# Kernel tuning notes

Measured on AMD Instinct MI355X. Metric: run time of the kernel, lower is better.

## Reference

```python
import jax, jax.numpy as jnp
import numpy as np

EMBED = 1024
HEADS = 16
HEAD_DIM = EMBED // HEADS
FFN = 4096
BSZ = 2
CHUNK = 128
NCHUNK = 16
REG_LEN = CHUNK * NCHUNK   # 2048
SUM_LEN = NCHUNK           # 1 summary token per chunk
NEG = -1e9


def _layer_norm(x, g, b, eps=1e-5):
    mu = x.mean(-1, keepdims=True)
    var = ((x - mu) ** 2).mean(-1, keepdims=True)
    return (x - mu) * jax.lax.rsqrt(var + eps) * g + b


def _build_mask(reg_chunk_ranges, sum_len, reg_len):
    # True = attention allowed. Museformer hierarchical scheme:
    #   rr: reg token attends reg tokens of its OWN chunk, causally
    #   rs: reg token attends summary tokens of STRICTLY EARLIER chunks
    #   sr: summary token of chunk c attends reg tokens of chunk c
    #   ss: causal among summary tokens
    bsz = reg_chunk_ranges.shape[0]
    starts = reg_chunk_ranges[:, :, 0]                       # [B, C]
    t = jnp.arange(reg_len)
    chunk_id = (t[None, :, None] >= starts[:, None, :]).sum(-1) - 1   # [B, R]
    sum_chunk = jnp.arange(sum_len)                          # [S]
    rr = (chunk_id[:, :, None] == chunk_id[:, None, :]) & (t[None, :, None] >= t[None, None, :])
    rs = sum_chunk[None, None, :] < chunk_id[:, :, None]     # [B, R, S]
    sr = chunk_id[:, None, :] == sum_chunk[None, :, None]    # [B, S, R]
    ss = jnp.broadcast_to(sum_chunk[:, None] >= sum_chunk[None, :], (bsz, sum_len, sum_len))
    top = jnp.concatenate([ss, sr], axis=2)
    bot = jnp.concatenate([rs, rr], axis=2)
    return jnp.concatenate([top, bot], axis=1)               # [B, S+R, S+R]


def _forward(x, w_q, w_k, w_v, w_o,
             ln_sa_sum_g, ln_sa_sum_b, ln_sa_reg_g, ln_sa_reg_b,
             sum_fc1_w, sum_fc1_b, sum_fc2_w, sum_fc2_b,
             reg_fc1_w, reg_fc1_b, reg_fc2_w, reg_fc2_b,
             ln_f_sum_g, ln_f_sum_b, ln_f_reg_g, ln_f_reg_b,
             reg_chunk_ranges, sum_len, reg_len):
    bsz, total, d = x.shape
    # --- self-attention block (pre-norm, separate LN for sum/reg parts) ---
    hs = _layer_norm(x[:, :sum_len], ln_sa_sum_g, ln_sa_sum_b)
    hr = _layer_norm(x[:, sum_len:], ln_sa_reg_g, ln_sa_reg_b)
    h = jnp.concatenate([hs, hr], axis=1)
    q = (h @ w_q.T).reshape(bsz, total, HEADS, HEAD_DIM)
    k = (h @ w_k.T).reshape(bsz, total, HEADS, HEAD_DIM)
    v = (h @ w_v.T).reshape(bsz, total, HEADS, HEAD_DIM)
    scores = jnp.einsum('bqhd,bkhd->bhqk', q, k) * (HEAD_DIM ** -0.5)
    mask = _build_mask(reg_chunk_ranges, sum_len, reg_len)   # [B, T, T] bool
    scores = jnp.where(mask[:, None], scores, NEG)
    attn = jax.nn.softmax(scores, axis=-1)
    ctx = jnp.einsum('bhqk,bkhd->bqhd', attn, v).reshape(bsz, total, d)
    x = x + ctx @ w_o.T
    # --- FFN block (pre-norm, separate LN/FFN for sum/reg parts) ---
    fs = _layer_norm(x[:, :sum_len], ln_f_sum_g, ln_f_sum_b)
    fs = jax.nn.relu(fs @ sum_fc1_w.T + sum_fc1_b) @ sum_fc2_w.T + sum_fc2_b
    fr = _layer_norm(x[:, sum_len:], ln_f_reg_g, ln_f_reg_b)
    fr = jax.nn.relu(fr @ reg_fc1_w.T + reg_fc1_b) @ reg_fc2_w.T + reg_fc2_b
    return x + jnp.concatenate([fs, fr], axis=1)


def setup_inputs() -> dict:
    key = jax.random.key(0)
    ks = jax.random.split(key, 12)
    s = 0.02
    total = SUM_LEN + REG_LEN
    starts = (np.arange(NCHUNK) * CHUNK).astype(np.int32)
    ranges = np.stack([starts, starts + CHUNK], axis=-1)     # [C, 2]
    reg_chunk_ranges = jnp.asarray(np.broadcast_to(ranges, (BSZ, NCHUNK, 2)).copy())
    d = dict(
        x=jax.random.normal(ks[0], (BSZ, total, EMBED), jnp.float32),
        w_q=jax.random.normal(ks[1], (EMBED, EMBED), jnp.float32) * s,
        w_k=jax.random.normal(ks[2], (EMBED, EMBED), jnp.float32) * s,
        w_v=jax.random.normal(ks[3], (EMBED, EMBED), jnp.float32) * s,
        w_o=jax.random.normal(ks[4], (EMBED, EMBED), jnp.float32) * s,
        ln_sa_sum_g=jnp.ones((EMBED,)), ln_sa_sum_b=jnp.zeros((EMBED,)),
        ln_sa_reg_g=jnp.ones((EMBED,)), ln_sa_reg_b=jnp.zeros((EMBED,)),
        sum_fc1_w=jax.random.normal(ks[5], (FFN, EMBED), jnp.float32) * s,
        sum_fc1_b=jnp.zeros((FFN,)),
        sum_fc2_w=jax.random.normal(ks[6], (EMBED, FFN), jnp.float32) * s,
        sum_fc2_b=jnp.zeros((EMBED,)),
        reg_fc1_w=jax.random.normal(ks[7], (FFN, EMBED), jnp.float32) * s,
        reg_fc1_b=jnp.zeros((FFN,)),
        reg_fc2_w=jax.random.normal(ks[8], (EMBED, FFN), jnp.float32) * s,
        reg_fc2_b=jnp.zeros((EMBED,)),
        ln_f_sum_g=jnp.ones((EMBED,)), ln_f_sum_b=jnp.zeros((EMBED,)),
        ln_f_reg_g=jnp.ones((EMBED,)), ln_f_reg_b=jnp.zeros((EMBED,)),
        reg_chunk_ranges=reg_chunk_ranges,
        sum_len=SUM_LEN,
        reg_len=REG_LEN,
    )
    return d


def reference(x, w_q, w_k, w_v, w_o,
              ln_sa_sum_g, ln_sa_sum_b, ln_sa_reg_g, ln_sa_reg_b,
              sum_fc1_w, sum_fc1_b, sum_fc2_w, sum_fc2_b,
              reg_fc1_w, reg_fc1_b, reg_fc2_w, reg_fc2_b,
              ln_f_sum_g, ln_f_sum_b, ln_f_reg_g, ln_f_reg_b,
              reg_chunk_ranges, sum_len, reg_len):
    return _forward(x, w_q, w_k, w_v, w_o,
                    ln_sa_sum_g, ln_sa_sum_b, ln_sa_reg_g, ln_sa_reg_b,
                    sum_fc1_w, sum_fc1_b, sum_fc2_w, sum_fc2_b,
                    reg_fc1_w, reg_fc1_b, reg_fc2_w, reg_fc2_b,
                    ln_f_sum_g, ln_f_sum_b, ln_f_reg_g, ln_f_reg_b,
                    reg_chunk_ranges, sum_len, reg_len)
```

## Files before the change

### kernel.cpp

```cpp
#include <hip/hip_runtime.h>
#include <stdint.h>

typedef __attribute__((ext_vector_type(8))) short short8;
typedef __attribute__((ext_vector_type(4))) float f32x4;

__device__ __forceinline__ float bf2f(short s) {
    union { unsigned u; float f; } c;
    c.u = ((unsigned)(unsigned short)s) << 16;
    return c.f;
}
__device__ __forceinline__ short f2bf(float f) {
    union { float f; unsigned u; } c; c.f = f;
    unsigned u = c.u + 0x7fffu + ((c.u >> 16) & 1u);
    return (short)(u >> 16);
}
__device__ __forceinline__ void gll16(const short* g, short* l) {
    __builtin_amdgcn_global_load_lds(
        (const __attribute__((address_space(1))) unsigned int*)g,
        (__attribute__((address_space(3))) unsigned int*)l, 16, 0, 0);
}

__global__ __launch_bounds__(256) void cvt_w(
    const float* __restrict__ wq, const float* __restrict__ wk,
    const float* __restrict__ wv, const float* __restrict__ wo,
    const float* __restrict__ f1s, const float* __restrict__ f2s,
    const float* __restrict__ f1r, const float* __restrict__ f2r,
    short* __restrict__ dst)
{
    size_t i = ((size_t)blockIdx.x * 256 + threadIdx.x) * 4;
    const float* src; size_t off;
    if (i < 4194304) {
        int seg = (int)(i >> 20);
        src = seg == 0 ? wq : seg == 1 ? wk : seg == 2 ? wv : wo;
        off = i & 1048575;
    } else {
        size_t ii = i - 4194304;
        int seg = (int)(ii >> 22);
        src = seg == 0 ? f1s : seg == 1 ? f2s : seg == 2 ? f1r : f2r;
        off = ii & 4194303;
    }
    float4 v = *(const float4*)(src + off);
    short4 o;
    o.x = f2bf(v.x); o.y = f2bf(v.y); o.z = f2bf(v.z); o.w = f2bf(v.w);
    *(short4*)(dst + i) = o;
}

template<int PHASE>
__global__ __launch_bounds__(256) void ln_k(
    const float* __restrict__ xin, const short* __restrict__ Pw, float* __restrict__ x1out,
    const float* __restrict__ g_sum, const float* __restrict__ b_sum,
    const float* __restrict__ g_reg, const float* __restrict__ b_reg,
    short* __restrict__ out_all, short* __restrict__ out_s, short* __restrict__ out_r)
{
    int row = blockIdx.x;
    int b = row / 2064, t = row - b * 2064;
    int tid = threadIdx.x;
    int c = tid * 4;
    size_t base = (size_t)row * 1024 + c;
    float4 v = *(const float4*)(xin + base);
    if (PHASE == 1) {
#pragma unroll
        for (int z = 0; z < 4; ++z) {
            short4 p = *(const short4*)(Pw + (size_t)z * 4227072 + base);
            v.x += bf2f(p.x); v.y += bf2f(p.y);
            v.z += bf2f(p.z); v.w += bf2f(p.w);
        }
        *(float4*)(x1out + base) = v;
    }
    float s = v.x + v.y + v.z + v.w;
#pragma unroll
    for (int off = 1; off < 64; off <<= 1) s += __shfl_xor(s, off);
    __shared__ float red[8];
    if ((tid & 63) == 0) red[tid >> 6] = s;
    __syncthreads();
    float mu = (red[0] + red[1] + red[2] + red[3]) * (1.0f / 1024.0f);
    float a0 = v.x - mu, a1 = v.y - mu, a2 = v.z - mu, a3 = v.w - mu;
    float qq = a0 * a0 + a1 * a1 + a2 * a2 + a3 * a3;
#pragma unroll
    for (int off = 1; off < 64; off <<= 1) qq += __shfl_xor(qq, off);
    if ((tid & 63) == 0) red[4 + (tid >> 6)] = qq;
    __syncthreads();
    float var = (red[4] + red[5] + red[6] + red[7]) * (1.0f / 1024.0f);
    float rs = rsqrtf(var + 1e-5f);
    const float* g  = (t < 16) ? g_sum : g_reg;
    const float* be = (t < 16) ? b_sum : b_reg;
    short4 o;
    o.x = f2bf(a0 * rs * g[c]     + be[c]);
    o.y = f2bf(a1 * rs * g[c + 1] + be[c + 1]);
    o.z = f2bf(a2 * rs * g[c + 2] + be[c + 2]);
    o.w = f2bf(a3 * rs * g[c + 3] + be[c + 3]);
    short* dst;
    if (PHASE == 0) dst = out_all + (size_t)row * 1024;
    else dst = (t < 16) ? (out_s + ((size_t)b * 16 + t) * 1024)
                        : (out_r + ((size_t)b * 2048 + (t - 16)) * 1024);
    *(short4*)(dst + c) = o;
}

template<int MODE>
__global__ __launch_bounds__(256) void gemm_bt(
    const short* __restrict__ A, int M, int K, int klen,
    const short* __restrict__ B0, const short* __restrict__ B1, const short* __restrict__ B2,
    const float* __restrict__ bias,
    void* __restrict__ o0, void* __restrict__ o1, void* __restrict__ o2, int seg)
{
    const int tid = threadIdx.x;
    const int w = tid >> 6, l = tid & 63;
    const int lr = l & 15, lh = l >> 4;
    const int m0 = blockIdx.x * 128;
    int ntile = blockIdx.y, nsel = 0;
    const short* B = B0;
    if (MODE == 0) { nsel = ntile >> 3; ntile &= 7; B = nsel == 0 ? B0 : (nsel == 1 ? B1 : B2); }
    const int n0 = ntile * 128;
    const int wr = (w >> 1) * 64, wc = (w & 1) * 64;
    const int kbase = blockIdx.z * klen;

    __shared__ __align__(16) short As[2 * 4096];
    __shared__ __align__(16) short Bs[2 * 4096];

    const int srow = w * 32 + (l >> 2);
    const int scol = (((l & 3) ^ ((l >> 3) & 3))) * 8;
    int ar0 = m0 + srow;      if (ar0 > M - 1) ar0 = M - 1;
    int ar1 = m0 + srow + 16; if (ar1 > M - 1) ar1 = M - 1;
    const short* ga0 = A + (size_t)ar0 * K + scol + kbase;
    const short* ga1 = A + (size_t)ar1 * K + scol + kbase;
    const short* gb0 = B + (size_t)(n0 + srow) * K + scol + kbase;
    const short* gb1 = B + (size_t)(n0 + srow + 16) * K + scol + kbase;
    const int lofs = (w * 32) * 32;

    const int cbrd = (lh ^ ((lr >> 1) & 3)) * 8;

    f32x4 acc[4][4];
#pragma unroll
    for (int m = 0; m < 4; ++m)
#pragma unroll
        for (int n = 0; n < 4; ++n) acc[m][n] = (f32x4){0.f, 0.f, 0.f, 0.f};

    auto STAGE = [&](int j, int buf) {
        const int k0 = j * 32;
        short* a = As + buf * 4096 + lofs;
        short* b = Bs + buf * 4096 + lofs;
        gll16(ga0 + k0, a);
        gll16(ga1 + k0, a + 512);
        gll16(gb0 + k0, b);
        gll16(gb1 + k0, b + 512);
    };

    const int nk = klen >> 5;
    STAGE(0, 0);
    for (int t = 0; t < nk; ++t) {
        __syncthreads();
        const int cur = (t & 1);
        if (t + 1 < nk) STAGE(t + 1, cur ^ 1);
        const int co = cur << 12;
        short8 af[4], bfr[4];
#pragma unroll
        for (int m = 0; m < 4; ++m)
            af[m] = *(const short8*)(As + co + (wr + m * 16 + lr) * 32 + cbrd);
#pragma unroll
        for (int n = 0; n < 4; ++n)
            bfr[n] = *(const short8*)(Bs + co + (wc + n * 16 + lr) * 32 + cbrd);
#pragma unroll
        for (int m = 0; m < 4; ++m)
#pragma unroll
            for (int n = 0; n < 4; ++n)
                acc[m][n] = __builtin_amdgcn_mfma_f32_16x16x32_bf16(af[m], bfr[n], acc[m][n], 0, 0, 0);
    }

#pragma unroll
    for (int m = 0; m < 4; ++m) {
#pragma unroll
        for (int n = 0; n < 4; ++n) {
            int gc = n0 + wc + n * 16 + lr;
#pragma unroll
            for (int j = 0; j < 4; ++j) {
                int gr = m0 + wr + m * 16 + lh * 4 + j;
                if (gr >= M) continue;
                float val = acc[m][n][j];
                if (MODE == 0) {
                    short* o = (short*)(nsel == 0 ? o0 : (nsel == 1 ? o1 : o2));
                    o[(size_t)gr * 1024 + gc] = f2bf(val);
                } else if (MODE == 1) {
                    float* P = (float*)o0 + (size_t)blockIdx.z * (size_t)seg;
                    P[(size_t)gr * 1024 + gc] = val;
                } else if (MODE == 2) {
                    val += bias[gc];
                    val = val > 0.f ? val : 0.f;
                    ((short*)o0)[(size_t)gr * 4096 + gc] = f2bf(val);
                } else {
                    short* P = (short*)o0 + (size_t)blockIdx.z * (size_t)seg;
                    P[(size_t)gr * 1024 + gc] = f2bf(val);
                }
            }
        }
    }
}

__global__ __launch_bounds__(256) void reduce_f2reg(
    const float* __restrict__ x1, const short* __restrict__ P,
    const float* __restrict__ bias, float* __restrict__ out)
{
    size_t i = ((size_t)blockIdx.x * 256 + threadIdx.x) * 4;
    int gr = (int)(i >> 10), c = (int)(i & 1023);
    size_t g = (size_t)((gr >> 11) * 2064 + 16 + (gr & 2047)) * 1024 + c;
    float4 r  = *(const float4*)(x1 + g);
    float4 bb = *(const float4*)(bias + c);
    float ox = r.x + bb.x, oy = r.y + bb.y, oz = r.z + bb.z, ow = r.w + bb.w;
#pragma unroll
    for (int z = 0; z < 4; ++z) {
        short4 p = *(const short4*)(P + (size_t)z * 4194304 + i);
        ox += bf2f(p.x); oy += bf2f(p.y); oz += bf2f(p.z); ow += bf2f(p.w);
    }
    float4 o; o.x = ox; o.y = oy; o.z = oz; o.w = ow;
    *(float4*)(out + g) = o;
}

__global__ __launch_bounds__(256) void reduce_f2sum(
    const float* __restrict__ x1, const float* __restrict__ P,
    const float* __restrict__ bias, float* __restrict__ out)
{
    int i = (blockIdx.x * 256 + threadIdx.x) * 4;
    int gr = i >> 10, c = i & 1023;
    size_t g = (size_t)((gr >> 4) * 2064 + (gr & 15)) * 1024 + c;
    float4 r  = *(const float4*)(x1 + g);
    float4 bb = *(const float4*)(bias + c);
    float ox = r.x + bb.x, oy = r.y + bb.y, oz = r.z + bb.z, ow = r.w + bb.w;
#pragma unroll
    for (int s = 0; s < 16; ++s) {
        float4 p = *(const float4*)(P + s * 32768 + i);
        ox += p.x; oy += p.y; oz += p.z; ow += p.w;
    }
    float4 o; o.x = ox; o.y = oy; o.z = oz; o.w = ow;
    *(float4*)(out + g) = o;
}

__global__ __launch_bounds__(256) void attn_reg(
    const short* __restrict__ q, const short* __restrict__ k,
    const short* __restrict__ v, short* __restrict__ ctx)
{
    __shared__ __align__(16) short Pl[128 * 168];
    __shared__ __align__(16) short Vt[64 * 168];
    short* Kl = Pl;

    const int tid = threadIdx.x;
    const int w = tid >> 6, l = tid & 63, lr = l & 15, lh = l >> 4;
    const int c = blockIdx.x, h = blockIdx.y, b = blockIdx.z;
    const int hc = h * 64;
    const size_t rowq0 = (size_t)b * 2064 + 16 + (size_t)c * 128;

    for (int ch = tid; ch < 1152; ch += 256) {
        int row = ch >> 3, kk = (ch & 7) << 3;
        size_t grow = (row < 16) ? ((size_t)b * 2064 + row) : (rowq0 + row - 16);
        *(int4*)(Kl + row * 72 + kk) = *(const int4*)(k + grow * 1024 + hc + kk);
    }
    for (int ch = tid; ch < 1152; ch += 256) {
        int j = ch % 144, db = ch / 144;
        size_t grow = (j < 16) ? ((size_t)b * 2064 + j) : (rowq0 + j - 16);
        short8 dv = *(const short8*)(v + grow * 1024 + hc + db * 8);
#pragma unroll
        for (int i = 0; i < 8; ++i) Vt[(db * 8 + i) * 168 + j] = dv[i];
    }
    for (int idx = tid; idx < 1024; idx += 256) {
        int d = idx >> 4, jj = 144 + (idx & 15);
        Vt[d * 168 + jj] = 0;
    }
    __syncthreads();

    short8 qf[2][2];
#pragma unroll
    for (int m = 0; m < 2; ++m) {
        size_t grow = rowq0 + w * 32 + m * 16 + lr;
#pragma unroll
        for (int ks = 0; ks < 2; ++ks)
            qf[m][ks] = *(const short8*)(q + grow * 1024 + hc + ks * 32 + lh * 8);
    }

    f32x4 s[2][9];
#pragma unroll
    for (int m = 0; m < 2; ++m)
#pragma unroll
        for (int n = 0; n < 9; ++n) s[m][n] = (f32x4){0.f, 0.f, 0.f, 0.f};
#pragma unroll
    for (int n = 0; n < 9; ++n) {
        const short* kr = Kl + (n * 16 + lr) * 72;
        short8 k0 = *(const short8*)(kr + lh * 8);
        short8 k1 = *(const short8*)(kr + 32 + lh * 8);
        s[0][n] = __builtin_amdgcn_mfma_f32_16x16x32_bf16(qf[0][0], k0, s[0][n], 0, 0, 0);
        s[0][n] = __builtin_amdgcn_mfma_f32_16x16x32_bf16(qf[0][1], k1, s[0][n], 0, 0, 0);
        s[1][n] = __builtin_amdgcn_mfma_f32_16x16x32_bf16(qf[1][0], k0, s[1][n], 0, 0, 0);
        s[1][n] = __builtin_amdgcn_mfma_f32_16x16x32_bf16(qf[1][1], k1, s[1][n], 0, 0, 0);
    }

    float inv_[2][4];
#pragma unroll
    for (int m = 0; m < 2; ++m) {
#pragma unroll
        for (int j = 0; j < 4; ++j) {
            int p = w * 32 + m * 16 + lh * 4 + j;
            float best = -1e30f;
            float e[9];
#pragma unroll
            for (int n = 0; n < 9; ++n) {
                int kk = n * 16 + lr;
                bool vis = (kk < 16) ? (kk < c) : (kk - 16 <= p);
                float val = vis ? s[m][n][j] * 0.125f : -1e30f;
                e[n] = val;
                best = fmaxf(best, val);
            }
#pragma unroll
            for (int off = 1; off < 16; off <<= 1) best = fmaxf(best, __shfl_xor(best, off));
            float sm = 0.f;
#pragma unroll
            for (int n = 0; n < 9; ++n) {
                float ex = __expf(e[n] - best);
                s[m][n][j] = ex;
                sm += ex;
            }
#pragma unroll
            for (int off = 1; off < 16; off <<= 1) sm += __shfl_xor(sm, off);
            inv_[m][j] = 1.0f / sm;
        }
    }

    __syncthreads();
#pragma unroll
    for (int m = 0; m < 2; ++m)
#pragma unroll
        for (int n = 0; n < 9; ++n)
#pragma unroll
            for (int j = 0; j < 4; ++j)
                Pl[(w * 32 + m * 16 + lh * 4 + j) * 168 + n * 16 + lr] = f2bf(s[m][n][j]);
    for (int idx = l; idx < 512; idx += 64) {
        int rr = idx >> 4, kkp = 144 + (idx & 15);
        Pl[(w * 32 + rr) * 168 + kkp] = 0;
    }
    __syncthreads();

    f32x4 dacc[2][4];
#pragma unroll
    for (int m = 0; m < 2; ++m)
#pragma unroll
        for (int n = 0; n < 4; ++n) dacc[m][n] = (f32x4){0.f, 0.f, 0.f, 0.f};
#pragma unroll
    for (int ks = 0; ks < 5; ++ks) {
        int kk0 = ks * 32;
        short8 pa[2];
#pragma unroll
        for (int m = 0; m < 2; ++m)
            pa[m] = *(const short8*)(Pl + (w * 32 + m * 16 + lr) * 168 + kk0 + lh * 8);
#pragma unroll
        for (int n = 0; n < 4; ++n) {
            short8 vb = *(const short8*)(Vt + (n * 16 + lr) * 168 + kk0 + lh * 8);
            dacc[0][n] = __builtin_amdgcn_mfma_f32_16x16x32_bf16(pa[0], vb, dacc[0][n], 0, 0, 0);
            dacc[1][n] = __builtin_amdgcn_mfma_f32_16x16x32_bf16(pa[1], vb, dacc[1][n], 0, 0, 0);
        }
    }

#pragma unroll
    for (int m = 0; m < 2; ++m)
#pragma unroll
        for (int n = 0; n < 4; ++n)
#pragma unroll
            for (int j = 0; j < 4; ++j) {
                int p = w * 32 + m * 16 + lh * 4 + j;
                ctx[(rowq0 + p) * 1024 + hc + n * 16 + lr] = f2bf(dacc[m][n][j] * inv_[m][j]);
            }
}

__global__ __launch_bounds__(64) void attn_sum(
    const short* __restrict__ q, const short* __restrict__ k,
    const short* __restrict__ v, short* __restrict__ ctx)
{
    int idx = blockIdx.x;
    int b = idx >> 8, h = (idx >> 4) & 15, s = idx & 15;
    int l = threadIdx.x;
    int hc = h * 64;
    size_t qrow = (size_t)b * 2064 + s;
    __shared__ float qv[64];
    __shared__ float pp[192];
    qv[l] = bf2f(q[qrow * 1024 + hc + l]);
    __syncthreads();
    float sc[3];
#pragma unroll
    for (int i = 0; i < 3; ++i) {
        int j = l + i * 64;
        float t = -1e30f;
        if (j < 144 && (j >= 16 || j <= s)) {
            size_t kr = (j < 16) ? ((size_t)b * 2064 + j)
                                 : ((size_t)b * 2064 + 16 + (size_t)s * 128 + (j - 16));
            const short* kp = k + kr * 1024 + hc;
            float acc = 0.f;
            for (int d = 0; d < 64; ++d) acc += qv[d] * bf2f(kp[d]);
            t = acc * 0.125f;
        }
        sc[i] = t;
    }
    float mx = fmaxf(sc[0], fmaxf(sc[1], sc[2]));
#pragma unroll
    for (int off = 1; off < 64; off <<= 1) mx = fmaxf(mx, __shfl_xor(mx, off));
    float sm = 0.f;
#pragma unroll
    for (int i = 0; i < 3; ++i) {
        float ex = (sc[i] > -1e29f) ? __expf(sc[i] - mx) : 0.f;
        pp[l + i * 64] = ex;
        sm += ex;
    }
#pragma unroll
    for (int off = 1; off < 64; off <<= 1) sm += __shfl_xor(sm, off);
    __syncthreads();
    float invs = 1.0f / sm;
    float acc = 0.f;
    for (int j = 0; j < 144; ++j) {
        float pj = pp[j];
        size_t vr = (j < 16) ? ((size_t)b * 2064 + j)
                             : ((size_t)b * 2064 + 16 + (size_t)s * 128 + (j - 16));
        acc += pj * bf2f(v[vr * 1024 + hc + l]);
    }
    ctx[qrow * 1024 + hc + l] = f2bf(acc * invs);
}

extern "C" void kernel_launch(void* const* d_in, const int* in_sizes, int n_in,
                              void* d_out, int out_size, void* d_ws, size_t ws_size,
                              hipStream_t stream) {
    const float* x    = (const float*)d_in[0];
    const float* wq   = (const float*)d_in[1];
    const float* wk   = (const float*)d_in[2];
    const float* wv   = (const float*)d_in[3];
    const float* wo   = (const float*)d_in[4];
    const float* lsg  = (const float*)d_in[5];
    const float* lsb  = (const float*)d_in[6];
    const float* lrg  = (const float*)d_in[7];
    const float* lrb  = (const float*)d_in[8];
    const float* sf1w = (const float*)d_in[9];
    const float* sf1b = (const float*)d_in[10];
    const float* sf2w = (const float*)d_in[11];
    const float* sf2b = (const float*)d_in[12];
    const float* rf1w = (const float*)d_in[13];
    const float* rf1b = (const float*)d_in[14];
    const float* rf2w = (const float*)d_in[15];
    const float* rf2b = (const float*)d_in[16];
    const float* fsg  = (const float*)d_in[17];
    const float* fsb  = (const float*)d_in[18];
    const float* frg  = (const float*)d_in[19];
    const float* frb  = (const float*)d_in[20];
    float* out = (float*)d_out;

    char* ws = (char*)d_ws;
    short* wbf   = (short*)ws;
    short* wq_b  = wbf;
    short* wk_b  = wbf + 1048576;
    short* wv_b  = wbf + 2097152;
    short* wo_b  = wbf + 3145728;
    short* f1s_b = wbf + 4194304;
    short* f2s_b = wbf + 8388608;
    short* f1r_b = wbf + 12582912;
    short* f2r_b = wbf + 16777216;
    short* h_all = (short*)(ws + 41943040);
    short* qb   = (short*)(ws + 50397184);
    short* kb   = qb + 4227072;
    short* vb   = kb + 4227072;
    short* ctxb = vb + 4227072;
    short* Pwo = (short*)(ws + 41943040);
    float* x1 = (float*)(ws + 84213760);
    short* h2_reg = (short*)ws;
    short* h2_sum = (short*)(ws + 75759616);
    short* f1_reg = (short*)(ws + 41943040);
    short* f1_sum = (short*)(ws + 75825152);
    float* Psum = (float*)(ws + 8388608);
    short* Pf2 = (short*)ws;

    cvt_w<<<20480, 256, 0, stream>>>(wq, wk, wv, wo, sf1w, sf2w, rf1w, rf2w, wbf);
    ln_k<0><<<4128, 256, 0, stream>>>(x, nullptr, nullptr, lsg, lsb, lrg, lrb,
                                      h_all, nullptr, nullptr);
    gemm_bt<0><<<dim3(33, 24, 1), 256, 0, stream>>>(h_all, 4128, 1024, 1024,
        wq_b, wk_b, wv_b, nullptr, qb, kb, vb, 0);
    attn_reg<<<dim3(16, 16, 2), 256, 0, stream>>>(qb, kb, vb, ctxb);
    attn_sum<<<512, 64, 0, stream>>>(qb, kb, vb, ctxb);
    gemm_bt<3><<<dim3(33, 8, 4), 256, 0, stream>>>(ctxb, 4128, 1024, 256,
        wo_b, nullptr, nullptr, nullptr, Pwo, nullptr, nullptr, 4227072);
    ln_k<1><<<4128, 256, 0, stream>>>(x, Pwo, x1, fsg, fsb, frg, frb,
                                      nullptr, h2_sum, h2_reg);
    gemm_bt<2><<<dim3(32, 32, 1), 256, 0, stream>>>(h2_reg, 4096, 1024, 1024,
        f1r_b, nullptr, nullptr, rf1b, f1_reg, nullptr, nullptr, 0);
    gemm_bt<2><<<dim3(1, 32, 1), 256, 0, stream>>>(h2_sum, 32, 1024, 1024,
        f1s_b, nullptr, nullptr, sf1b, f1_sum, nullptr, nullptr, 0);
    gemm_bt<1><<<dim3(1, 8, 16), 256, 0, stream>>>(f1_sum, 32, 4096, 256,
        f2s_b, nullptr, nullptr, nullptr, Psum, nullptr, nullptr, 32768);
    reduce_f2sum<<<32, 256, 0, stream>>>(x1, Psum, sf2b, out);
    gemm_bt<3><<<dim3(32, 8, 4), 256, 0, stream>>>(f1_reg, 4096, 4096, 1024,
        f2r_b, nullptr, nullptr, nullptr, Pf2, nullptr, nullptr, 4194304);
    reduce_f2reg<<<4096, 256, 0, stream>>>(x1, Pf2, rf2b, out);
}
```

Before: 310.4 us.

## Add 256x256-tile 512-thread GEMM for the large projections and FFN matmuls

Adds a gemm256 kernel with 256x256 output tiles: 8 waves per block, each computing a 128x64 sub-tile, with double-buffered 64KB of LDS. It replaces the 128x128 GEMM for the QKV, output-projection, FFN1-reg and FFN2-reg matmuls, which roughly doubles operand reuse per LDS load. The old kernel is slimmed down and kept only for the tiny summary-token GEMMs. The cost is that block counts fall to about 200–270 on a 256-CU part, so occupancy drops to one block per CU. The extra M-padding on the 4128-row matrices also adds some wasted work.

```diff
diff --git a/kernel.cpp b/kernel.cpp
--- a/kernel.cpp
+++ b/kernel.cpp
@@ -97,7 +97,7 @@
 }
 
 template<int MODE>
-__global__ __launch_bounds__(256) void gemm_bt(
+__global__ __launch_bounds__(512) void gemm256(
     const short* __restrict__ A, int M, int K, int klen,
     const short* __restrict__ B0, const short* __restrict__ B1, const short* __restrict__ B2,
     const float* __restrict__ bias,
@@ -106,16 +106,16 @@
     const int tid = threadIdx.x;
     const int w = tid >> 6, l = tid & 63;
     const int lr = l & 15, lh = l >> 4;
-    const int m0 = blockIdx.x * 128;
+    const int m0 = blockIdx.x * 256;
     int ntile = blockIdx.y, nsel = 0;
     const short* B = B0;
-    if (MODE == 0) { nsel = ntile >> 3; ntile &= 7; B = nsel == 0 ? B0 : (nsel == 1 ? B1 : B2); }
-    const int n0 = ntile * 128;
-    const int wr = (w >> 1) * 64, wc = (w & 1) * 64;
+    if (MODE == 0) { nsel = ntile >> 2; ntile &= 3; B = nsel == 0 ? B0 : (nsel == 1 ? B1 : B2); }
+    const int n0 = ntile * 256;
+    const int wm = w >> 2, wn = w & 3;
     const int kbase = blockIdx.z * klen;
 
-    __shared__ __align__(16) short As[2 * 4096];
-    __shared__ __align__(16) short Bs[2 * 4096];
+    __shared__ __align__(16) short As[2 * 8192];
+    __shared__ __align__(16) short Bs[2 * 8192];
 
     const int srow = w * 32 + (l >> 2);
     const int scol = (((l & 3) ^ ((l >> 3) & 3))) * 8;
@@ -129,6 +129,98 @@
 
     const int cbrd = (lh ^ ((lr >> 1) & 3)) * 8;
 
+    f32x4 acc[8][4];
+#pragma unroll
+    for (int m = 0; m < 8; ++m)
+#pragma unroll
+        for (int n = 0; n < 4; ++n) acc[m][n] = (f32x4){0.f, 0.f, 0.f, 0.f};
+
+    auto STAGE = [&](int j, int buf) {
+        const int k0 = j * 32;
+        short* a = As + buf * 8192 + lofs;
+        short* b = Bs + buf * 8192 + lofs;
+        gll16(ga0 + k0, a);
+        gll16(ga1 + k0, a + 512);
+        gll16(gb0 + k0, b);
+        gll16(gb1 + k0, b + 512);
+    };
+
+    const int nk = klen >> 5;
+    STAGE(0, 0);
+    for (int t = 0; t < nk; ++t) {
+        __syncthreads();
+        const int cur = (t & 1);
+        if (t + 1 < nk) STAGE(t + 1, cur ^ 1);
+        const int co = cur << 13;
+        short8 bfr[4];
+#pragma unroll
+        for (int n = 0; n < 4; ++n)
+            bfr[n] = *(const short8*)(Bs + co + (wn * 64 + n * 16 + lr) * 32 + cbrd);
+#pragma unroll
+        for (int m = 0; m < 8; ++m) {
+            short8 af = *(const short8*)(As + co + (wm * 128 + m * 16 + lr) * 32 + cbrd);
+#pragma unroll
+            for (int n = 0; n < 4; ++n)
+                acc[m][n] = __builtin_amdgcn_mfma_f32_16x16x32_bf16(af, bfr[n], acc[m][n], 0, 0, 0);
+        }
+    }
+
+#pragma unroll
+    for (int m = 0; m < 8; ++m) {
+#pragma unroll
+        for (int n = 0; n < 4; ++n) {
+            int gc = n0 + wn * 64 + n * 16 + lr;
+#pragma unroll
+            for (int j = 0; j < 4; ++j) {
+                int gr = m0 + wm * 128 + m * 16 + lh * 4 + j;
+                if (gr >= M) continue;
+                float val = acc[m][n][j];
+                if (MODE == 0) {
+                    short* o = (short*)(nsel == 0 ? o0 : (nsel == 1 ? o1 : o2));
+                    o[(size_t)gr * 1024 + gc] = f2bf(val);
+                } else if (MODE == 2) {
+                    val += bias[gc];
+                    val = val > 0.f ? val : 0.f;
+                    ((short*)o0)[(size_t)gr * 4096 + gc] = f2bf(val);
+                } else {
+                    short* P = (short*)o0 + (size_t)blockIdx.z * (size_t)seg;
+                    P[(size_t)gr * 1024 + gc] = f2bf(val);
+                }
+            }
+        }
+    }
+}
+
+template<int MODE>
+__global__ __launch_bounds__(256) void gemm_bt(
+    const short* __restrict__ A, int M, int K, int klen,
+    const short* __restrict__ B0,
+    const float* __restrict__ bias,
+    void* __restrict__ o0, int seg)
+{
+    const int tid = threadIdx.x;
+    const int w = tid >> 6, l = tid & 63;
+    const int lr = l & 15, lh = l >> 4;
+    const int m0 = blockIdx.x * 128;
+    const int n0 = blockIdx.y * 128;
+    const short* B = B0;
+    const int wr = (w >> 1) * 64, wc = (w & 1) * 64;
+    const int kbase = blockIdx.z * klen;
+
+    __shared__ __align__(16) short As[2 * 4096];
+    __shared__ __align__(16) short Bs[2 * 4096];
+
+    const int srow = w * 32 + (l >> 2);
+    const int scol = (((l & 3) ^ ((l >> 3) & 3))) * 8;
+    int ar0 = m0 + srow;      if (ar0 > M - 1) ar0 = M - 1;
+    int ar1 = m0 + srow + 16; if (ar1 > M - 1) ar1 = M - 1;
+    const short* ga0 = A + (size_t)ar0 * K + scol + kbase;
+    const short* ga1 = A + (size_t)ar1 * K + scol + kbase;
+    const short* gb0 = B + (size_t)(n0 + srow) * K + scol + kbase;
+    const short* gb1 = B + (size_t)(n0 + srow + 16) * K + scol + kbase;
+    const int lofs = (w * 32) * 32;
+    const int cbrd = (lh ^ ((lr >> 1) & 3)) * 8;
+
     f32x4 acc[4][4];
 #pragma unroll
     for (int m = 0; m < 4; ++m)
@@ -176,19 +268,13 @@
                 int gr = m0 + wr + m * 16 + lh * 4 + j;
                 if (gr >= M) continue;
                 float val = acc[m][n][j];
-                if (MODE == 0) {
-                    short* o = (short*)(nsel == 0 ? o0 : (nsel == 1 ? o1 : o2));
-                    o[(size_t)gr * 1024 + gc] = f2bf(val);
-                } else if (MODE == 1) {
+                if (MODE == 1) {
                     float* P = (float*)o0 + (size_t)blockIdx.z * (size_t)seg;
                     P[(size_t)gr * 1024 + gc] = val;
-                } else if (MODE == 2) {
+                } else {
                     val += bias[gc];
                     val = val > 0.f ? val : 0.f;
                     ((short*)o0)[(size_t)gr * 4096 + gc] = f2bf(val);
-                } else {
-                    short* P = (short*)o0 + (size_t)blockIdx.z * (size_t)seg;
-                    P[(size_t)gr * 1024 + gc] = f2bf(val);
                 }
             }
         }
@@ -459,34 +545,34 @@
     short* kb   = qb + 4227072;
     short* vb   = kb + 4227072;
     short* ctxb = vb + 4227072;
-    short* Pwo = (short*)(ws + 41943040);
-    float* x1 = (float*)(ws + 84213760);
+    short* Pwo  = (short*)(ws + 41943040);
+    float* x1   = (float*)(ws + 84213760);
     short* h2_reg = (short*)ws;
     short* h2_sum = (short*)(ws + 75759616);
     short* f1_reg = (short*)(ws + 41943040);
     short* f1_sum = (short*)(ws + 75825152);
-    float* Psum = (float*)(ws + 8388608);
-    short* Pf2 = (short*)ws;
+    float* Psum   = (float*)(ws + 8388608);
+    short* Pf2    = (short*)ws;
 
     cvt_w<<<20480, 256, 0, stream>>>(wq, wk, wv, wo, sf1w, sf2w, rf1w, rf2w, wbf);
     ln_k<0><<<4128, 256, 0, stream>>>(x, nullptr, nullptr, lsg, lsb, lrg, lrb,
                                       h_all, nullptr, nullptr);
-    gemm_bt<0><<<dim3(33, 24, 1), 256, 0, stream>>>(h_all, 4128, 1024, 1024,
+    gemm256<0><<<dim3(17, 12, 1), 512, 0, stream>>>(h_all, 4128, 1024, 1024,
         wq_b, wk_b, wv_b, nullptr, qb, kb, vb, 0);
     attn_reg<<<dim3(16, 16, 2), 256, 0, stream>>>(qb, kb, vb, ctxb);
     attn_sum<<<512, 64, 0, stream>>>(qb, kb, vb, ctxb);
-    gemm_bt<3><<<dim3(33, 8, 4), 256, 0, stream>>>(ctxb, 4128, 1024, 256,
+    gemm256<3><<<dim3(17, 4, 4), 512, 0, stream>>>(ctxb, 4128, 1024, 256,
         wo_b, nullptr, nullptr, nullptr, Pwo, nullptr, nullptr, 4227072);
     ln_k<1><<<4128, 256, 0, stream>>>(x, Pwo, x1, fsg, fsb, frg, frb,
                                       nullptr, h2_sum, h2_reg);
-    gemm_bt<2><<<dim3(32, 32, 1), 256, 0, stream>>>(h2_reg, 4096, 1024, 1024,
+    gemm256<2><<<dim3(16, 16, 1), 512, 0, stream>>>(h2_reg, 4096, 1024, 1024,
         f1r_b, nullptr, nullptr, rf1b, f1_reg, nullptr, nullptr, 0);
     gemm_bt<2><<<dim3(1, 32, 1), 256, 0, stream>>>(h2_sum, 32, 1024, 1024,
-        f1s_b, nullptr, nullptr, sf1b, f1_sum, nullptr, nullptr, 0);
+        f1s_b, sf1b, f1_sum, 0);
     gemm_bt<1><<<dim3(1, 8, 16), 256, 0, stream>>>(f1_sum, 32, 4096, 256,
-        f2s_b, nullptr, nullptr, nullptr, Psum, nullptr, nullptr, 32768);
+        f2s_b, nullptr, Psum, 32768);
     reduce_f2sum<<<32, 256, 0, stream>>>(x1, Psum, sf2b, out);
-    gemm_bt<3><<<dim3(32, 8, 4), 256, 0, stream>>>(f1_reg, 4096, 4096, 1024,
+    gemm256<3><<<dim3(16, 4, 4), 512, 0, stream>>>(f1_reg, 4096, 4096, 1024,
         f2r_b, nullptr, nullptr, nullptr, Pf2, nullptr, nullptr, 4194304);
     reduce_f2reg<<<4096, 256, 0, stream>>>(x1, Pf2, rf2b, out);
 }
```

Result: no change. 315.3 us (+1.6%).
